# Kernel optimization log

Measured on AMD Instinct MI355X. Metric: run time of the kernel, lower is better.

## Reference

```python
import jax, jax.numpy as jnp
import numpy as np

B, N, K1, M, D = 8, 4096, 17, 2, 256
NT = B * N          # total nodes
EPS = 1e-5          # PyG LayerNorm default eps


def setup_inputs() -> dict:
    key = jax.random.key(0)
    ks = jax.random.split(key, 13)
    s = 1.0 / np.sqrt(D)
    return {
        "x": jax.random.normal(ks[0], (NT, M, D), jnp.float32),
        "knn_edges": jax.random.randint(ks[1], (B, N, K1), 0, N),
        "edge_mask": jax.random.bernoulli(ks[2], 0.9, (B, N, K1)),
        "W0": jax.random.normal(ks[3], (D, D), jnp.float32) * s,
        "b0": jnp.zeros((D,), jnp.float32),
        "g0": jnp.ones((D,), jnp.float32),
        "be0": jnp.zeros((D,), jnp.float32),
        "a0": jnp.full((1,), 0.25, jnp.float32),
        "W1": jax.random.normal(ks[4], (D, D), jnp.float32) * s,
        "b1": jnp.zeros((D,), jnp.float32),
        "g1": jnp.ones((D,), jnp.float32),
        "be1": jnp.zeros((D,), jnp.float32),
        "a1": jnp.full((1,), 0.25, jnp.float32),
    }


def knn_to_edges(knn_edges, edge_mask):
    # drop self column 0, add per-graph batch offsets; keep fixed E with 0/1 weights
    e = knn_edges[:, :, 1:]                       # [B, N, K]
    m = edge_mask[:, :, 1:]
    off = (jnp.arange(B) * N)[:, None, None]      # [B,1,1]
    src = jnp.broadcast_to(jnp.arange(N)[None, :, None] + off, e.shape).reshape(-1)
    dst = (e + off).reshape(-1)
    w = m.reshape(-1).astype(jnp.float32)         # invalid edges -> weight 0
    return src, dst, w


def gcn_conv(h_in, W, b, src, dst, w):
    # PyG GCNConv: add self-loops (weight 1), symmetric normalization
    h = h_in @ W                                            # [NT, D]
    deg = jax.ops.segment_sum(w, dst, num_segments=NT) + 1.0
    dinv = jax.lax.rsqrt(deg)                               # [NT]
    norm = dinv[src] * w * dinv[dst]                        # [E]
    agg = jax.ops.segment_sum(norm[:, None] * h[src], dst, num_segments=NT)
    agg = agg + (dinv * dinv)[:, None] * h                  # self-loop term
    return agg + b


def graph_layernorm(x, g, b):
    # PyG LayerNorm mode='graph', batch=None: normalize over all nodes+features
    xc = x - jnp.mean(x)
    std = jnp.sqrt(jnp.mean(xc * xc))
    return g * (xc / (std + EPS)) + b


def prelu(x, a):
    return jnp.where(x >= 0, x, a * x)


def reference(x, knn_edges, edge_mask, W0, b0, g0, be0, a0, W1, b1, g1, be1, a1):
    src, dst, w = knn_to_edges(knn_edges, edge_mask)
    h = x[:, 0, :]                                          # [NT, D]
    for (W, b, g, be, a) in ((W0, b0, g0, be0, a0), (W1, b1, g1, be1, a1)):
        h = gcn_conv(h, W, b, src, dst, w)
        h = graph_layernorm(h, g, be)
        h = prelu(h, a)
    return h
```

## Files before the change

kernel.cpp:

```cpp
#include <hip/hip_runtime.h>
#include <hip/hip_bf16.h>
#include <stdint.h>

#define B_   8
#define N_   4096
#define K1_  17
#define D_   256
#define NT_  (B_*N_)
#define E16_ (NT_*16)
#define NP_  (NT_*D_)
#define EPS_ 1e-5f

typedef __attribute__((ext_vector_type(8))) short short8v;
typedef __attribute__((ext_vector_type(4))) short short4v;
typedef __attribute__((ext_vector_type(4))) float f32x4;

__device__ __forceinline__ unsigned short f2bfu(float f){
  unsigned u = __float_as_uint(f);
  unsigned r = (u + 0x7FFFu + ((u>>16)&1u)) >> 16;
  return (unsigned short)r;
}
__device__ __forceinline__ short f2bf(float f){ return (short)f2bfu(f); }
__device__ __forceinline__ unsigned pkbf(float lo, float hi){
  return (unsigned)f2bfu(lo) | ((unsigned)f2bfu(hi) << 16);
}
__device__ __forceinline__ float bf2f(short s){
  return __uint_as_float(((unsigned)(unsigned short)s) << 16);
}
__device__ __forceinline__ void unpack2(unsigned u, float& lo, float& hi){
  lo = __uint_as_float(u << 16);
  hi = __uint_as_float(u & 0xFFFF0000u);
}

__global__ __launch_bounds__(256) void k_prep(const float* __restrict__ W0,
                                              const float* __restrict__ W1,
                                              short* __restrict__ Wt0,
                                              short* __restrict__ Wt1,
                                              int* __restrict__ degcnt,
                                              const unsigned int* __restrict__ mw,
                                              int* __restrict__ flag){
  if (blockIdx.x < 128){
    const float* W  = (blockIdx.x & 1) ? W1  : W0;
    short*       Wt = (blockIdx.x & 1) ? Wt1 : Wt0;
    int tile = blockIdx.x >> 1;
    int ti = tile >> 3, tj = tile & 7;
    __shared__ float sm[32][33];
    int r = threadIdx.x >> 5, c = threadIdx.x & 31;
    #pragma unroll
    for (int i=0;i<4;i++)
      sm[r + i*8][c] = W[(ti*32 + r + i*8)*256 + tj*32 + c];
    __syncthreads();
    #pragma unroll
    for (int i=0;i<4;i++){
      int rr = r + i*8;
      Wt[(size_t)(tj*32 + rr)*256 + ti*32 + c] = f2bf(sm[c][rr]);
    }
  } else {
    int ib = blockIdx.x - 128;
    int i  = ib*256 + threadIdx.x;
    degcnt[i] = 0;
    if (ib == 0){
      __shared__ int s_int, s_f32;
      if (threadIdx.x==0){ s_int=1; s_f32=1; }
      __syncthreads();
      int bad_i=0, bad_f=0;
      #pragma unroll
      for (int j=0;j<4;j++){
        unsigned w = mw[threadIdx.x*4 + j];
        if (!(w==0u || w==1u))          bad_i=1;
        if (!(w==0u || w==0x3F800000u)) bad_f=1;
      }
      if (bad_i) atomicAnd(&s_int, 0);
      if (bad_f) atomicAnd(&s_f32, 0);
      __syncthreads();
      if (threadIdx.x==0) *flag = s_int ? 0 : (s_f32 ? 1 : 2);
    }
  }
}

__device__ __forceinline__ bool mask_at(const void* maskp, int f, int idx){
  if (f==0) return ((const int*)maskp)[idx] != 0;
  if (f==1) return ((const float*)maskp)[idx] != 0.0f;
  return ((const unsigned char*)maskp)[idx] != 0;
}

__global__ void k_deg(const int* __restrict__ knn, const void* __restrict__ maskp,
                      const int* __restrict__ flag, int* __restrict__ degcnt){
  int f = *flag;
  int e = blockIdx.x*blockDim.x + threadIdx.x;
  if (e >= E16_) return;
  int node = e >> 4;
  int k    = (e & 15) + 1;
  int idx  = node*K1_ + k;
  if (mask_at(maskp, f, idx)){
    int b   = node >> 12;
    int dst = knn[idx] + (b<<12);
    atomicAdd(&degcnt[dst], 1);
  }
}

__global__ void k_scan(const int* __restrict__ degcnt, int* __restrict__ rowptr,
                       int* __restrict__ fillptr, float* __restrict__ dinv){
  __shared__ int sm[1024];
  int t = threadIdx.x;
  int base = t*32;
  int loc[32]; int tot = 0;
  #pragma unroll
  for (int i=0;i<32;i++){ loc[i] = degcnt[base+i]; tot += loc[i]; }
  sm[t] = tot; __syncthreads();
  for (int off=1; off<1024; off<<=1){
    int v = (t>=off) ? sm[t-off] : 0;
    __syncthreads();
    sm[t] += v;
    __syncthreads();
  }
  int run = sm[t] - tot;
  #pragma unroll
  for (int i=0;i<32;i++){
    int v = base+i;
    rowptr[v]  = run;
    fillptr[v] = run;
    dinv[v]    = rsqrtf((float)loc[i] + 1.0f);
    run += loc[i];
  }
  if (t==1023) rowptr[NT_] = run;
}

__global__ void k_fill(const int* __restrict__ knn, const void* __restrict__ maskp,
                       const int* __restrict__ flag, int* __restrict__ fillptr,
                       int* __restrict__ col){
  int f = *flag;
  int e = blockIdx.x*blockDim.x + threadIdx.x;
  if (e >= E16_) return;
  int node = e >> 4;
  int k    = (e & 15) + 1;
  int idx  = node*K1_ + k;
  if (mask_at(maskp, f, idx)){
    int b   = node >> 12;
    int dst = knn[idx] + (b<<12);
    int pos = atomicAdd(&fillptr[dst], 1);
    col[pos] = node;
  }
}


__global__ __launch_bounds__(256, 3) void k_gemm_x(const float* __restrict__ X,
                                                   const short* __restrict__ Wt,
                                                   short* __restrict__ C){
  __shared__ short lA[128*64];
  __shared__ short lB[128*64];
  int lb     = (int)(blockIdx.x & 7)*64 + (int)(blockIdx.x >> 3);
  int rowblk = lb >> 1, half = lb & 1;
  int rowB = rowblk*128, colB = half*128;

  int t    = threadIdx.x;
  int wave = t >> 6, lane = t & 63;
  int lr   = lane & 15, qg = lane >> 4;
  int wr   = wave >> 1, wc = wave & 1;

  f32x4 acc[4][4];
  #pragma unroll
  for (int m=0;m<4;m++)
    #pragma unroll
    for (int n=0;n<4;n++) acc[m][n] = (f32x4){0.f,0.f,0.f,0.f};

  int srow[4], sch[4];
  #pragma unroll
  for (int i=0;i<4;i++){ int e = t + i*256; srow[i] = e>>3; sch[i] = e&7; }

  float4 rax[4], ray[4]; uint4 rb[4];
  #pragma unroll
  for (int i=0;i<4;i++){
    const float* ap = X + (size_t)(rowB+srow[i])*512 + sch[i]*8;
    rax[i] = *(const float4*)ap;
    ray[i] = *(const float4*)(ap+4);
    rb[i]  = *(const uint4*)(Wt + (size_t)(colB+srow[i])*256 + sch[i]*8);
  }

  for (int kc=0; kc<4; kc++){
    if (kc) __syncthreads();
    #pragma unroll
    for (int i=0;i<4;i++){
      int ph = srow[i]*8 + (sch[i] ^ (srow[i]&7));
      uint4 cv;
      cv.x = pkbf(rax[i].x, rax[i].y); cv.y = pkbf(rax[i].z, rax[i].w);
      cv.z = pkbf(ray[i].x, ray[i].y); cv.w = pkbf(ray[i].z, ray[i].w);
      *(uint4*)(lA + ph*8) = cv;
      *(uint4*)(lB + ph*8) = rb[i];
    }
    __syncthreads();
    if (kc < 3){
      #pragma unroll
      for (int i=0;i<4;i++){
        const float* ap = X + (size_t)(rowB+srow[i])*512 + (kc+1)*64 + sch[i]*8;
        rax[i] = *(const float4*)ap;
        ray[i] = *(const float4*)(ap+4);
        rb[i]  = *(const uint4*)(Wt + (size_t)(colB+srow[i])*256 + (kc+1)*64 + sch[i]*8);
      }
    }
    #pragma unroll
    for (int ks=0; ks<2; ks++){
      short8v af[4], bfr[4];
      #pragma unroll
      for (int m=0;m<4;m++){
        int row = wr*64 + m*16 + lr;
        af[m] = *(const short8v*)(lA + (row*8 + ((ks*4+qg) ^ (row&7)))*8);
      }
      #pragma unroll
      for (int n=0;n<4;n++){
        int coln = wc*64 + n*16 + lr;
        bfr[n] = *(const short8v*)(lB + (coln*8 + ((ks*4+qg) ^ (coln&7)))*8);
      }
      #pragma unroll
      for (int m=0;m<4;m++)
        #pragma unroll
        for (int n=0;n<4;n++)
          acc[m][n] = __builtin_amdgcn_mfma_f32_16x16x32_bf16(af[m], bfr[n], acc[m][n], 0, 0, 0);
    }
  }

  #pragma unroll
  for (int m=0;m<4;m++){
    int crow = rowB + wr*64 + m*16 + qg*4;
    #pragma unroll
    for (int n=0;n<4;n++){
      int ccol = colB + wc*64 + n*16 + lr;
      #pragma unroll
      for (int r=0;r<4;r++)
        C[(size_t)(crow + r)*256 + ccol] = f2bf(acc[m][n][r]);
    }
  }
}

__global__ __launch_bounds__(256, 3) void k_gemm_n(const unsigned* __restrict__ BaggU,
                                                   const float* __restrict__ g,
                                                   const float* __restrict__ be,
                                                   const float* __restrict__ aP,
                                                   const float* __restrict__ stats,
                                                   const short* __restrict__ Wt,
                                                   short* __restrict__ C){
  float mean = stats[0], inv = stats[1], a = aP[0];
  __shared__ short lA[128*64];
  __shared__ short lB[128*64];
  int lb     = (int)(blockIdx.x & 7)*64 + (int)(blockIdx.x >> 3);
  int rowblk = lb >> 1, half = lb & 1;
  int rowB = rowblk*128, colB = half*128;

  int t    = threadIdx.x;
  int wave = t >> 6, lane = t & 63;
  int lr   = lane & 15, qg = lane >> 4;
  int wr   = wave >> 1, wc = wave & 1;

  f32x4 acc[4][4];
  #pragma unroll
  for (int m=0;m<4;m++)
    #pragma unroll
    for (int n=0;n<4;n++) acc[m][n] = (f32x4){0.f,0.f,0.f,0.f};

  int srow[4], sch[4];
  #pragma unroll
  for (int i=0;i<4;i++){ int e = t + i*256; srow[i] = e>>3; sch[i] = e&7; }

  uint4 ra[4], rb[4];
  #pragma unroll
  for (int i=0;i<4;i++){
    ra[i] = *(const uint4*)(BaggU + (size_t)(rowB+srow[i])*128 + sch[i]*4);
    rb[i] = *(const uint4*)(Wt + (size_t)(colB+srow[i])*256 + sch[i]*8);
  }

  for (int kc=0; kc<4; kc++){
    if (kc) __syncthreads();
    #pragma unroll
    for (int i=0;i<4;i++){
      int ph = srow[i]*8 + (sch[i] ^ (srow[i]&7));
      int c0 = kc*64 + sch[i]*8;
      float4 g0 = *(const float4*)&g[c0],  g1 = *(const float4*)&g[c0+4];
      float4 e0 = *(const float4*)&be[c0], e1 = *(const float4*)&be[c0+4];
      float v[8];
      unpack2(ra[i].x, v[0], v[1]); unpack2(ra[i].y, v[2], v[3]);
      unpack2(ra[i].z, v[4], v[5]); unpack2(ra[i].w, v[6], v[7]);
      float gg[8] = {g0.x,g0.y,g0.z,g0.w,g1.x,g1.y,g1.z,g1.w};
      float eb[8] = {e0.x,e0.y,e0.z,e0.w,e1.x,e1.y,e1.z,e1.w};
      float o[8];
      #pragma unroll
      for (int j=0;j<8;j++){
        float tt = gg[j]*((v[j]-mean)*inv) + eb[j];
        o[j] = tt>=0.f ? tt : a*tt;
      }
      uint4 cv;
      cv.x = pkbf(o[0],o[1]); cv.y = pkbf(o[2],o[3]);
      cv.z = pkbf(o[4],o[5]); cv.w = pkbf(o[6],o[7]);
      *(uint4*)(lA + ph*8) = cv;
      *(uint4*)(lB + ph*8) = rb[i];
    }
    __syncthreads();
    if (kc < 3){
      #pragma unroll
      for (int i=0;i<4;i++){
        ra[i] = *(const uint4*)(BaggU + (size_t)(rowB+srow[i])*128 + (kc+1)*32 + sch[i]*4);
        rb[i] = *(const uint4*)(Wt + (size_t)(colB+srow[i])*256 + (kc+1)*64 + sch[i]*8);
      }
    }
    #pragma unroll
    for (int ks=0; ks<2; ks++){
      short8v af[4], bfr[4];
      #pragma unroll
      for (int m=0;m<4;m++){
        int row = wr*64 + m*16 + lr;
        af[m] = *(const short8v*)(lA + (row*8 + ((ks*4+qg) ^ (row&7)))*8);
      }
      #pragma unroll
      for (int n=0;n<4;n++){
        int coln = wc*64 + n*16 + lr;
        bfr[n] = *(const short8v*)(lB + (coln*8 + ((ks*4+qg) ^ (coln&7)))*8);
      }
      #pragma unroll
      for (int m=0;m<4;m++)
        #pragma unroll
        for (int n=0;n<4;n++)
          acc[m][n] = __builtin_amdgcn_mfma_f32_16x16x32_bf16(af[m], bfr[n], acc[m][n], 0, 0, 0);
    }
  }

  #pragma unroll
  for (int m=0;m<4;m++){
    int crow = rowB + wr*64 + m*16 + qg*4;
    #pragma unroll
    for (int n=0;n<4;n++){
      int ccol = colB + wc*64 + n*16 + lr;
      #pragma unroll
      for (int r=0;r<4;r++)
        C[(size_t)(crow + r)*256 + ccol] = f2bf(acc[m][n][r]);
    }
  }
}

__global__ __launch_bounds__(256) void k_agg(const short* __restrict__ Ab,
    const int* __restrict__ rowptr, const int* __restrict__ col,
    const float* __restrict__ dinv, const float* __restrict__ bvec,
    unsigned* __restrict__ outU, float* __restrict__ partS, float* __restrict__ partQ){
  int bid  = (int)(blockIdx.x & 7) * 512 + (int)(blockIdx.x >> 3);
  int node = bid*8 + (threadIdx.x >> 5);
  int sub  = threadIdx.x & 31;
  int c0   = sub*8;
  float dv = dinv[node];

  float acc[8];
  {
    short8v s = *(const short8v*)&Ab[(size_t)node*256 + c0];
    #pragma unroll
    for (int i=0;i<8;i++) acc[i] = dv * bf2f(s[i]);
  }
  int j0 = rowptr[node], j1 = rowptr[node+1];
  for (int base=j0; base<j1; base+=32){
    int n = j1 - base; n = n < 32 ? n : 32;
    int   myc = (sub < n) ? col[base+sub] : 0;
    float myd = (sub < n) ? dinv[myc]     : 0.f;
    for (int j=0;j<n;j++){
      int   s  = __shfl(myc, j, 32);
      float ds = __shfl(myd, j, 32);
      short8v nb = *(const short8v*)&Ab[(size_t)s*256 + c0];
      #pragma unroll
      for (int i=0;i<8;i++) acc[i] += ds * bf2f(nb[i]);
    }
  }
  float sum=0.f, sq=0.f;
  float o[8];
  #pragma unroll
  for (int i=0;i<8;i++){
    float v = dv*acc[i] + bvec[c0+i];
    o[i] = v;
    sum += v; sq += v*v;
  }
  uint4 ov;
  ov.x = pkbf(o[0],o[1]); ov.y = pkbf(o[2],o[3]);
  ov.z = pkbf(o[4],o[5]); ov.w = pkbf(o[6],o[7]);
  *(uint4*)&outU[(size_t)node*128 + sub*4] = ov;

  #pragma unroll
  for (int off=16; off>0; off>>=1){
    sum += __shfl_down(sum, off, 32);
    sq  += __shfl_down(sq,  off, 32);
  }
  __shared__ float ls1[8], ls2[8];
  if (sub==0){ ls1[threadIdx.x>>5]=sum; ls2[threadIdx.x>>5]=sq; }
  __syncthreads();
  if (threadIdx.x==0){
    float a=0.f, b=0.f;
    #pragma unroll
    for (int i=0;i<8;i++){ a+=ls1[i]; b+=ls2[i]; }
    partS[bid]=a; partQ[bid]=b;
  }
}

__global__ void k_stats(const float* __restrict__ partS, const float* __restrict__ partQ,
                        float* __restrict__ stats){
  __shared__ double s1[1024], s2[1024];
  int t = threadIdx.x;
  double a=0.0, b=0.0;
  for (int i=t; i<4096; i+=1024){ a += (double)partS[i]; b += (double)partQ[i]; }
  s1[t]=a; s2[t]=b; __syncthreads();
  for (int off=512; off>0; off>>=1){
    if (t<off){ s1[t]+=s1[t+off]; s2[t]+=s2[t+off]; }
    __syncthreads();
  }
  if (t==0){
    double mean = s1[0] / (double)NP_;
    double var  = s2[0] / (double)NP_ - mean*mean;
    var = var > 0.0 ? var : 0.0;
    stats[0] = (float)mean;
    stats[1] = (float)(1.0 / (sqrt(var) + (double)EPS_));
  }
}

__global__ __launch_bounds__(256) void k_norm_f32(const unsigned* __restrict__ inU,
    const float* __restrict__ g, const float* __restrict__ be,
    const float* __restrict__ aP, const float* __restrict__ stats,
    float* __restrict__ out){
  float mean = stats[0], inv = stats[1], a = aP[0];
  int gid   = blockIdx.x*256 + threadIdx.x;
  int base8 = gid*8;
  int c0    = base8 & (D_-1);
  uint4 vin = *(const uint4*)&inU[gid*4];
  float4 g0 = *(const float4*)&g[c0],  g1 = *(const float4*)&g[c0+4];
  float4 e0 = *(const float4*)&be[c0], e1 = *(const float4*)&be[c0+4];
  float v[8];
  unpack2(vin.x, v[0], v[1]); unpack2(vin.y, v[2], v[3]);
  unpack2(vin.z, v[4], v[5]); unpack2(vin.w, v[6], v[7]);
  float gg[8] = {g0.x,g0.y,g0.z,g0.w,g1.x,g1.y,g1.z,g1.w};
  float eb[8] = {e0.x,e0.y,e0.z,e0.w,e1.x,e1.y,e1.z,e1.w};
  f32x4 o0, o1;
  #pragma unroll
  for (int i=0;i<8;i++){
    float tt = gg[i]*((v[i]-mean)*inv) + eb[i];
    tt = tt>=0.f ? tt : a*tt;
    if (i<4) o0[i] = tt; else o1[i-4] = tt;
  }
  *(f32x4*)&out[base8]     = o0;
  *(f32x4*)&out[base8 + 4] = o1;
}


extern "C" void kernel_launch(void* const* d_in, const int* in_sizes, int n_in,
                              void* d_out, int out_size, void* d_ws, size_t ws_size,
                              hipStream_t stream){
  const float* x    = (const float*)d_in[0];
  const int*   knn  = (const int*)  d_in[1];
  const void*  mask =               d_in[2];
  const float* W0   = (const float*)d_in[3];
  const float* b0   = (const float*)d_in[4];
  const float* g0   = (const float*)d_in[5];
  const float* be0  = (const float*)d_in[6];
  const float* a0   = (const float*)d_in[7];
  const float* W1   = (const float*)d_in[8];
  const float* b1   = (const float*)d_in[9];
  const float* g1   = (const float*)d_in[10];
  const float* be1  = (const float*)d_in[11];
  const float* a1   = (const float*)d_in[12];
  float* out = (float*)d_out;

  char* w = (char*)d_ws;
  size_t off = 0;
  auto alloc = [&](size_t bytes)->void*{
    void* p = w + off; off = (off + bytes + 255) & ~(size_t)255; return p;
  };
  int*      degcnt  = (int*)     alloc(NT_*4);
  int*      rowptr  = (int*)     alloc((NT_+1)*4);
  int*      fillptr = (int*)     alloc(NT_*4);
  int*      col     = (int*)     alloc(E16_*4);
  float*    dinv    = (float*)   alloc(NT_*4);
  float*    partS   = (float*)   alloc(4096*4);
  float*    partQ   = (float*)   alloc(4096*4);
  float*    stats   = (float*)   alloc(4*4);
  int*      flag    = (int*)     alloc(4);
  short*    Ab      = (short*)   alloc((size_t)NP_*2);
  unsigned* Bagg    = (unsigned*)alloc((size_t)NP_*2);
  short*    Wt0     = (short*)   alloc(256*256*2);
  short*    Wt1     = (short*)   alloc(256*256*2);

  hipLaunchKernelGGL(k_prep,  dim3(256),      dim3(256), 0, stream, W0, W1, Wt0, Wt1,
                     degcnt, (const unsigned int*)mask, flag);
  hipLaunchKernelGGL(k_deg,   dim3(E16_/256), dim3(256), 0, stream, knn, mask, flag, degcnt);
  hipLaunchKernelGGL(k_scan,  dim3(1),        dim3(1024),0, stream, degcnt, rowptr, fillptr, dinv);
  hipLaunchKernelGGL(k_fill,  dim3(E16_/256), dim3(256), 0, stream, knn, mask, flag, fillptr, col);

  hipLaunchKernelGGL(k_gemm_x, dim3(512),     dim3(256), 0, stream, x, Wt0, Ab);
  hipLaunchKernelGGL(k_agg,    dim3(NT_/8),   dim3(256), 0, stream, Ab, rowptr, col, dinv, b0, Bagg, partS, partQ);
  hipLaunchKernelGGL(k_stats,  dim3(1),       dim3(1024),0, stream, partS, partQ, stats);

  hipLaunchKernelGGL(k_gemm_n, dim3(512),     dim3(256), 0, stream, Bagg, g0, be0, a0, stats, Wt1, Ab);
  hipLaunchKernelGGL(k_agg,    dim3(NT_/8),   dim3(256), 0, stream, Ab, rowptr, col, dinv, b1, Bagg, partS, partQ);
  hipLaunchKernelGGL(k_stats,  dim3(1),       dim3(1024),0, stream, partS, partQ, stats);
  hipLaunchKernelGGL(k_norm_f32, dim3(NP_/2048), dim3(256), 0, stream, Bagg, g1, be1, a1, stats, out);
}
```

Before: 166.4 us.

## Merge CSR fill into first GEMM launch and use wave-shuffle scan

```diff
diff --git a/kernel.cpp b/kernel.cpp
--- a/kernel.cpp
+++ b/kernel.cpp
@@ -101,20 +101,25 @@
 
 __global__ void k_scan(const int* __restrict__ degcnt, int* __restrict__ rowptr,
                        int* __restrict__ fillptr, float* __restrict__ dinv){
-  __shared__ int sm[1024];
+  __shared__ int wsum[16];
   int t = threadIdx.x;
+  int lane = t & 63, wid = t >> 6;
   int base = t*32;
   int loc[32]; int tot = 0;
   #pragma unroll
   for (int i=0;i<32;i++){ loc[i] = degcnt[base+i]; tot += loc[i]; }
-  sm[t] = tot; __syncthreads();
-  for (int off=1; off<1024; off<<=1){
-    int v = (t>=off) ? sm[t-off] : 0;
-    __syncthreads();
-    sm[t] += v;
-    __syncthreads();
-  }
-  int run = sm[t] - tot;
+  int inc = tot;
+  #pragma unroll
+  for (int off=1; off<64; off<<=1){
+    int v = __shfl_up(inc, off, 64);
+    if (lane >= off) inc += v;
+  }
+  if (lane == 63) wsum[wid] = inc;
+  __syncthreads();
+  int woff = 0;
+  #pragma unroll
+  for (int i=0;i<16;i++) if (i < wid) woff += wsum[i];
+  int run = woff + inc - tot;
   #pragma unroll
   for (int i=0;i<32;i++){
     int v = base+i;
@@ -126,29 +131,30 @@
   if (t==1023) rowptr[NT_] = run;
 }
 
-__global__ void k_fill(const int* __restrict__ knn, const void* __restrict__ maskp,
-                       const int* __restrict__ flag, int* __restrict__ fillptr,
-                       int* __restrict__ col){
-  int f = *flag;
-  int e = blockIdx.x*blockDim.x + threadIdx.x;
-  if (e >= E16_) return;
-  int node = e >> 4;
-  int k    = (e & 15) + 1;
-  int idx  = node*K1_ + k;
-  if (mask_at(maskp, f, idx)){
-    int b   = node >> 12;
-    int dst = knn[idx] + (b<<12);
-    int pos = atomicAdd(&fillptr[dst], 1);
-    col[pos] = node;
-  }
-}
-
-
-__global__ __launch_bounds__(256, 3) void k_gemm_x(const float* __restrict__ X,
-                                                   const short* __restrict__ Wt,
-                                                   short* __restrict__ C){
+__global__ __launch_bounds__(256, 3) void k_gemm_x_fill(const float* __restrict__ X,
+                                                        const short* __restrict__ Wt,
+                                                        short* __restrict__ C,
+                                                        const int* __restrict__ knn,
+                                                        const void* __restrict__ maskp,
+                                                        const int* __restrict__ flag,
+                                                        int* __restrict__ fillptr,
+                                                        int* __restrict__ col){
   __shared__ short lA[128*64];
   __shared__ short lB[128*64];
+  if (blockIdx.x >= 512){
+    int f = *flag;
+    int e = (blockIdx.x - 512)*256 + threadIdx.x;
+    int node = e >> 4;
+    int k    = (e & 15) + 1;
+    int idx  = node*K1_ + k;
+    if (mask_at(maskp, f, idx)){
+      int b   = node >> 12;
+      int dst = knn[idx] + (b<<12);
+      int pos = atomicAdd(&fillptr[dst], 1);
+      col[pos] = node;
+    }
+    return;
+  }
   int lb     = (int)(blockIdx.x & 7)*64 + (int)(blockIdx.x >> 3);
   int rowblk = lb >> 1, half = lb & 1;
   int rowB = rowblk*128, colB = half*128;
@@ -482,9 +488,9 @@
                      degcnt, (const unsigned int*)mask, flag);
   hipLaunchKernelGGL(k_deg,   dim3(E16_/256), dim3(256), 0, stream, knn, mask, flag, degcnt);
   hipLaunchKernelGGL(k_scan,  dim3(1),        dim3(1024),0, stream, degcnt, rowptr, fillptr, dinv);
-  hipLaunchKernelGGL(k_fill,  dim3(E16_/256), dim3(256), 0, stream, knn, mask, flag, fillptr, col);
-
-  hipLaunchKernelGGL(k_gemm_x, dim3(512),     dim3(256), 0, stream, x, Wt0, Ab);
+
+  hipLaunchKernelGGL(k_gemm_x_fill, dim3(2560), dim3(256), 0, stream, x, Wt0, Ab,
+                     knn, mask, flag, fillptr, col);
   hipLaunchKernelGGL(k_agg,    dim3(NT_/8),   dim3(256), 0, stream, Ab, rowptr, col, dinv, b0, Bagg, partS, partQ);
   hipLaunchKernelGGL(k_stats,  dim3(1),       dim3(1024),0, stream, partS, partQ, stats);
 
```

Result: faster. 159.8 us (-4.0%).
